# Kernel tuning notes

Measured on AMD Instinct MI355X. Metric: run time of the kernel, lower is better.

The kernel has to match this reference:

```python
import jax, jax.numpy as jnp
import numpy as np

NUM_HEADS = 12
NUM_LANDMARKS = 64


def iterative_inv(K, n_iter=6):
    # K: [B, H, L, L]; Newton-Schulz-style pseudo-inverse iteration
    I = jnp.eye(K.shape[-1], dtype=K.dtype)
    denom = jnp.max(jnp.sum(K, axis=-2), axis=-1)[..., None, None]  # [B,H,1,1]
    V = jnp.swapaxes(K, -1, -2) / denom
    for _ in range(n_iter):
        KV = K @ V
        V = 0.25 * V @ (13.0 * I - KV @ (15.0 * I - KV @ (7.0 * I - KV)))
    return V


def setup_inputs() -> dict:
    key = jax.random.key(0)
    k1, k2, k3, k4 = jax.random.split(key, 4)
    B, N, C = 8, 4096, 768
    x = jax.random.normal(k1, (B, N, C), dtype=jnp.float32)
    w_qkv = jax.random.normal(k2, (C, 3 * C), dtype=jnp.float32) * 0.02
    w_proj = jax.random.normal(k3, (C, C), dtype=jnp.float32) * 0.02
    b_proj = jax.random.normal(k4, (C,), dtype=jnp.float32) * 0.02
    return {"x": x, "w_qkv": w_qkv, "w_proj": w_proj, "b_proj": b_proj}


def reference(x, w_qkv, w_proj, b_proj):
    B, N, C = x.shape
    H, L = NUM_HEADS, NUM_LANDMARKS
    D = C // H
    scale = D ** 0.5

    qkv = (x @ w_qkv).reshape(B, N, 3, H, D)
    qkv = jnp.transpose(qkv, (2, 0, 3, 1, 4))  # [3, B, H, N, D]
    Q, K, V = qkv[0] / scale, qkv[1], qkv[2]

    segs = N // L  # r == 0 path (N divisible by L)
    K_lm = K.reshape(B, H, L, segs, D).mean(axis=-2)  # [B,H,L,D]
    Q_lm = Q.reshape(B, H, L, segs, D).mean(axis=-2)

    kernel1 = jax.nn.softmax(jnp.einsum('bhnd,bhld->bhnl', Q, K_lm), axis=-1)   # [B,H,N,L]
    kernel2 = jax.nn.softmax(jnp.einsum('bhld,bhmd->bhlm', Q_lm, K_lm), axis=-1)  # [B,H,L,L]
    kernel3 = jax.nn.softmax(jnp.einsum('bhld,bhnd->bhln', Q_lm, K), axis=-1)   # [B,H,L,N]

    SV = (kernel1 @ iterative_inv(kernel2)) @ (kernel3 @ V)  # [B,H,N,D]

    SV = jnp.transpose(SV, (0, 2, 1, 3)).reshape(B, N, C)
    out = SV @ w_proj + b_proj
    out = out + jnp.transpose(V, (0, 2, 1, 3)).reshape(B, N, C)
    return out
```

## Files before the change

kernel.cpp:

```cpp
#include <hip/hip_runtime.h>
#include <math.h>

#define BB   8
#define NN   4096
#define CC   768
#define HH   12
#define DD   64
#define LL   64
#define BH   96
#define MM_  32768
#define KQKV 768
#define NQKV 2304
#define NTILES 24

typedef short bf16x8 __attribute__((ext_vector_type(8)));
typedef float f32x4  __attribute__((ext_vector_type(4)));

union U4 { unsigned long long ll; unsigned short s[4]; };

__device__ __forceinline__ unsigned short f2bf(float f) {
  union { float f; unsigned u; } v; v.f = f;
  return (unsigned short)((v.u + 0x7FFFu + ((v.u >> 16) & 1u)) >> 16);
}
__device__ __forceinline__ float bf2f(unsigned short h) {
  union { unsigned u; float f; } v; v.u = ((unsigned)h) << 16;
  return v.f;
}
__device__ __forceinline__ f32x4 fzero4() {
  f32x4 z; z[0] = 0.f; z[1] = 0.f; z[2] = 0.f; z[3] = 0.f; return z;
}
__device__ __forceinline__ void gload_lds16(const void* g, void* l) {
  __builtin_amdgcn_global_load_lds(
      (const __attribute__((address_space(1))) void*)g,
      (__attribute__((address_space(3))) void*)l, 16, 0, 0);
}

__global__ void conv_bf16(const float* __restrict__ in, short* __restrict__ out, int n4) {
  int i = blockIdx.x * 256 + threadIdx.x;
  if (i >= n4) return;
  float4 v = ((const float4*)in)[i];
  U4 p; p.s[0] = f2bf(v.x); p.s[1] = f2bf(v.y); p.s[2] = f2bf(v.z); p.s[3] = f2bf(v.w);
  ((unsigned long long*)out)[i] = p.ll;
}

__global__ __launch_bounds__(256) void transpose_bf16(
    const float* __restrict__ in, short* __restrict__ out, int R, int C) {
  __shared__ float tile[32][33];
  int c0 = blockIdx.x * 32, r0 = blockIdx.y * 32;
  int tx = threadIdx.x & 31, ty = threadIdx.x >> 5;
  for (int i = ty; i < 32; i += 8)
    tile[i][tx] = in[(r0 + i) * C + c0 + tx];
  __syncthreads();
  for (int i = ty; i < 32; i += 8)
    out[(c0 + i) * R + r0 + tx] = (short)f2bf(tile[tx][i]);
}

template <int EPI>
__global__ __launch_bounds__(256, 3) void gemm128(
    const short* __restrict__ A, const short* __restrict__ Bw,
    short* __restrict__ o0, short* __restrict__ o1, short* __restrict__ o2,
    const float* __restrict__ bias, float* __restrict__ fout,
    short* __restrict__ Qlmb, short* __restrict__ Klmb,
    float* __restrict__ QlmF, float* __restrict__ KlmF) {
  __shared__ short L[24576];
  const int t = threadIdx.x;
  const int wave = t >> 6, lane = t & 63;
  const int wr = (wave >> 1) << 6, wc = (wave & 1) << 6;
  const int lrow = lane & 15, g = lane >> 4;

  const int q8 = gridDim.x >> 3;
  const int wg = ((int)blockIdx.x & 7) * q8 + ((int)blockIdx.x >> 3);
  const int NT = (EPI == 0) ? 18 : 6;
  const int tn = wg % NT, tm = wg / NT;
  const int m0 = tm << 7;

  const int csl = (((t & 3) ^ ((t >> 3) & 3)) << 3);
  const short* pA0 = A  + (size_t)(m0 + (t >> 2)) * KQKV + csl;
  const short* pA1 = pA0 + 64 * KQKV;
  const short* pB0 = Bw + (size_t)(tn * 128 + (t >> 2)) * KQKV + csl;
  const short* pB1 = pB0 + 64 * KQKV;
  char* dA = (char*)L + t * 16;
  char* dB = (char*)L + 8192 + t * 16;

  const int swz = ((g ^ ((lrow >> 1) & 3)) << 4);
  const int aoff = (wr + lrow) * 64 + swz;
  const int boff = 8192 + (wc + lrow) * 64 + swz;

  f32x4 acc[4][4];
#pragma unroll
  for (int i = 0; i < 4; ++i)
#pragma unroll
    for (int j = 0; j < 4; ++j) acc[i][j] = fzero4();

#pragma unroll
  for (int T = 0; T < 2; ++T) {
    gload_lds16(pA0 + T * 32, dA + T * 16384);
    gload_lds16(pA1 + T * 32, dA + T * 16384 + 4096);
    gload_lds16(pB0 + T * 32, dB + T * 16384);
    gload_lds16(pB1 + T * 32, dB + T * 16384 + 4096);
  }
  asm volatile("s_waitcnt vmcnt(4)" ::: "memory");
  __builtin_amdgcn_s_barrier();

  for (int T = 0; T < NTILES; ++T) {
    const int Ts = T + 2;
    if (Ts < NTILES) {
      const int sb = (Ts % 3) * 16384;
      gload_lds16(pA0 + Ts * 32, dA + sb);
      gload_lds16(pA1 + Ts * 32, dA + sb + 4096);
      gload_lds16(pB0 + Ts * 32, dB + sb);
      gload_lds16(pB1 + Ts * 32, dB + sb + 4096);
    }
    const char* Lb = (const char*)L + (T % 3) * 16384;
    bf16x8 a[4], b[4];
#pragma unroll
    for (int nf = 0; nf < 4; ++nf) b[nf] = *(const bf16x8*)(Lb + boff + nf * 1024);
#pragma unroll
    for (int rf = 0; rf < 4; ++rf) a[rf] = *(const bf16x8*)(Lb + aoff + rf * 1024);
#pragma unroll
    for (int rf = 0; rf < 4; ++rf)
#pragma unroll
      for (int nf = 0; nf < 4; ++nf)
        acc[rf][nf] = __builtin_amdgcn_mfma_f32_16x16x32_bf16(a[rf], b[nf], acc[rf][nf], 0, 0, 0);
    if (T < NTILES - 2)       { asm volatile("s_waitcnt vmcnt(4)" ::: "memory"); }
    else if (T == NTILES - 2) { asm volatile("s_waitcnt vmcnt(0)" ::: "memory"); }
    __builtin_amdgcn_s_barrier();
  }

  if constexpr (EPI == 0) {
    const int cg0 = tn * 128;
    const int three = cg0 / 768;
    const int ccb = cg0 % 768;
    short* dst = (three == 0) ? o0 : (three == 1) ? o1 : o2;
    const float sc = (three == 0) ? 0.125f : 1.f;
    short* LS = (short*)L;
#pragma unroll
    for (int rf = 0; rf < 4; ++rf)
#pragma unroll
      for (int nf = 0; nf < 4; ++nf)
#pragma unroll
        for (int i = 0; i < 4; ++i)
          LS[(wr + rf * 16 + g * 4 + i) * 144 + wc + nf * 16 + lrow] =
              (short)f2bf(acc[rf][nf][i] * sc);
    __syncthreads();
#pragma unroll
    for (int k = 0; k < 8; ++k) {
      int id = t + k * 256;
      int row = id >> 4, ch = id & 15;
      bf16x8 v = *(const bf16x8*)&LS[row * 144 + ch * 8];
      int c = ccb + ch * 8, h = c >> 6, d = c & 63;
      int r = m0 + row, bb = r >> 12, n = r & 4095;
      *(bf16x8*)&dst[((size_t)(bb * HH + h) * NN + n) * DD + d] = v;
    }
    if (three < 2) {
      int seg = t >> 7, col = t & 127;
      float ssum = 0.f;
#pragma unroll
      for (int j = 0; j < 64; ++j) ssum += bf2f((unsigned short)LS[(seg * 64 + j) * 144 + col]);
      ssum *= (1.f / 64.f);
      int l = ((tm & 31) << 1) + seg;
      int c = ccb + col, h = c >> 6, d = c & 63;
      int bh = (tm >> 5) * HH + h;
      int idx = bh * 4096 + l * 64 + d;
      if (three == 0) { QlmF[idx] = ssum; Qlmb[idx] = (short)f2bf(ssum); }
      else            { KlmF[idx] = ssum; Klmb[idx] = (short)f2bf(ssum); }
    }
  } else {
    float* LF = (float*)L;
#pragma unroll
    for (int pass = 0; pass < 2; ++pass) {
      if ((wave >> 1) == pass) {
#pragma unroll
        for (int rf = 0; rf < 4; ++rf)
#pragma unroll
          for (int nf = 0; nf < 4; ++nf)
#pragma unroll
            for (int i = 0; i < 4; ++i)
              LF[(rf * 16 + g * 4 + i) * 136 + wc + nf * 16 + lrow] = acc[rf][nf][i];
      }
      __syncthreads();
#pragma unroll
      for (int k = 0; k < 8; ++k) {
        int id = t + k * 256;
        int row = id >> 5, ch = id & 31;
        float4 v = *(const float4*)&LF[row * 136 + ch * 4];
        int R = m0 + pass * 64 + row;
        int c = tn * 128 + ch * 4;
        int bb = R >> 12, n = R & 4095, h = c >> 6, d = c & 63;
        float4 bi = *(const float4*)&bias[c];
        U4 r4;
        r4.ll = *(const unsigned long long*)&o2[((size_t)(bb * HH + h) * NN + n) * DD + d];
        v.x += bi.x + bf2f(r4.s[0]);
        v.y += bi.y + bf2f(r4.s[1]);
        v.z += bi.z + bf2f(r4.s[2]);
        v.w += bi.w + bf2f(r4.s[3]);
        *(float4*)&fout[(size_t)R * CC + c] = v;
      }
      __syncthreads();
    }
  }
}

__global__ __launch_bounds__(256) void e12(
    const short* __restrict__ Kb, const short* __restrict__ Vb,
    const short* __restrict__ Qlmb,
    float* __restrict__ k3VTp, float* __restrict__ s3part) {
  int bh = blockIdx.y, chunk = blockIdx.x;
  __shared__ short Qlm[64 * 72];
  __shared__ short Plds[64 * 136];
  __shared__ short Vl[128 * 68];
  int t = threadIdx.x;
  for (int r = 0; r < 2; r++) {
    int e = t + r * 256;
    *(bf16x8*)&Qlm[(e >> 3) * 72 + (e & 7) * 8] = *(const bf16x8*)&Qlmb[bh * 4096 + e * 8];
  }
  int wave = t >> 6, lane = t & 63, lrow = lane & 15, g = lane >> 4, lk = g << 3;
  f32x4 o2[4];
  float cpl[4];
#pragma unroll
  for (int lf = 0; lf < 4; lf++) { o2[lf] = fzero4(); cpl[lf] = 0.f; }
  const int dloc = wave * 16 + lrow;

  for (int s = 0; s < 4; ++s) {
    int nb = chunk * 512 + s * 128;
    __syncthreads();
#pragma unroll
    for (int r = 0; r < 4; r++) {
      int id = t + r * 256;
      int n = id >> 3, c8 = id & 7;
      unsigned long long v1 = *(const unsigned long long*)&Vb[((size_t)bh * NN + nb + n) * DD + c8 * 8];
      unsigned long long v2 = *(const unsigned long long*)&Vb[((size_t)bh * NN + nb + n) * DD + c8 * 8 + 4];
      *(unsigned long long*)&Vl[n * 68 + c8 * 8] = v1;
      *(unsigned long long*)&Vl[n * 68 + c8 * 8 + 4] = v2;
    }
    int nw = nb + wave * 32;
    bf16x8 aK[2][2];
#pragma unroll
    for (int rf = 0; rf < 2; rf++)
#pragma unroll
      for (int ks = 0; ks < 2; ks++)
        aK[rf][ks] = *(const bf16x8*)&Kb[((size_t)bh * NN + nw + rf * 16 + lrow) * DD + ks * 32 + lk];
    f32x4 acc[2][4];
#pragma unroll
    for (int rf = 0; rf < 2; rf++)
#pragma unroll
      for (int lf = 0; lf < 4; lf++) acc[rf][lf] = fzero4();
#pragma unroll
    for (int ks = 0; ks < 2; ks++) {
      bf16x8 bq[4];
#pragma unroll
      for (int lf = 0; lf < 4; lf++)
        bq[lf] = *(const bf16x8*)&Qlm[(lf * 16 + lrow) * 72 + ks * 32 + lk];
#pragma unroll
      for (int rf = 0; rf < 2; rf++)
#pragma unroll
        for (int lf = 0; lf < 4; lf++)
          acc[rf][lf] = __builtin_amdgcn_mfma_f32_16x16x32_bf16(aK[rf][ks], bq[lf], acc[rf][lf], 0, 0, 0);
    }
#pragma unroll
    for (int lf = 0; lf < 4; lf++) {
      int l = lf * 16 + lrow;
#pragma unroll
      for (int rf = 0; rf < 2; rf++) {
        U4 p;
#pragma unroll
        for (int i = 0; i < 4; i++) {
          float e = expf(acc[rf][lf][i]);
          p.s[i] = f2bf(e); cpl[lf] += e;
        }
        *(unsigned long long*)&Plds[l * 136 + wave * 32 + rf * 16 + g * 4] = p.ll;
      }
    }
    __syncthreads();
#pragma unroll
    for (int ks = 0; ks < 4; ++ks) {
      bf16x8 a;
#pragma unroll
      for (int j = 0; j < 8; ++j) a[j] = Vl[(ks * 32 + lk + j) * 68 + dloc];
#pragma unroll
      for (int lf = 0; lf < 4; lf++) {
        bf16x8 b = *(const bf16x8*)&Plds[(lf * 16 + lrow) * 136 + ks * 32 + lk];
        o2[lf] = __builtin_amdgcn_mfma_f32_16x16x32_bf16(a, b, o2[lf], 0, 0, 0);
      }
    }
  }
#pragma unroll
  for (int lf = 0; lf < 4; lf++) {
    float cp = cpl[lf];
    cp += __shfl_xor(cp, 16);
    cp += __shfl_xor(cp, 32);
    if (lane < 16)
      s3part[((bh * 8 + chunk) * 4 + wave) * LL + lf * 16 + lane] = cp;
    int l = lf * 16 + lrow;
#pragma unroll
    for (int i = 0; i < 4; i++) {
      int dd = wave * 16 + g * 4 + i;
      k3VTp[((size_t)chunk * BH + bh) * 4096 + dd * 64 + l] = o2[lf][i];
    }
  }
}

__device__ __forceinline__ void mm64(const float* X, const float* Y, int row, int c0, float o[8]) {
#pragma unroll
  for (int j = 0; j < 8; j++) o[j] = 0.f;
  for (int k = 0; k < 64; k++) {
    float x = X[row * 68 + k];
    const float4* yp = (const float4*)&Y[k * 68 + c0];
    float4 y0 = yp[0], y1 = yp[1];
    o[0] += x * y0.x; o[1] += x * y0.y; o[2] += x * y0.z; o[3] += x * y0.w;
    o[4] += x * y1.x; o[5] += x * y1.y; o[6] += x * y1.z; o[7] += x * y1.w;
  }
}

__global__ __launch_bounds__(512) void newton_inv(
    const float* __restrict__ QlmF, const float* __restrict__ KlmF,
    const float* __restrict__ k3VTp, const float* __restrict__ s3part,
    short* __restrict__ MTws) {
  __shared__ float A_[64 * 68], B_[64 * 68], C_[64 * 68], D_[64 * 68], E_[64 * 68];
  __shared__ float red[64];
  __shared__ float denom_s;
  int bh = blockIdx.x, t = threadIdx.x;
  int row = t >> 3, c0 = (t & 7) << 3;
#pragma unroll
  for (int i = 0; i < 8; i++) {
    int e = t * 8 + i;
    A_[(e >> 6) * 68 + (e & 63)] = QlmF[bh * 4096 + e];
    B_[(e >> 6) * 68 + (e & 63)] = KlmF[bh * 4096 + e];
  }
  __syncthreads();
  {
    float4 ar[16];
#pragma unroll
    for (int q = 0; q < 16; q++) ar[q] = *(const float4*)&A_[row * 68 + q * 4];
    float o[8];
#pragma unroll
    for (int mm = 0; mm < 8; mm++) {
      const float4* br = (const float4*)&B_[(c0 + mm) * 68];
      float s = 0.f;
      for (int q = 0; q < 16; q++) {
        float4 b4 = br[q];
        s += ar[q].x * b4.x + ar[q].y * b4.y + ar[q].z * b4.z + ar[q].w * b4.w;
      }
      o[mm] = s;
    }
    float mx = o[0];
#pragma unroll
    for (int mm = 1; mm < 8; mm++) mx = fmaxf(mx, o[mm]);
    mx = fmaxf(mx, __shfl_xor(mx, 1));
    mx = fmaxf(mx, __shfl_xor(mx, 2));
    mx = fmaxf(mx, __shfl_xor(mx, 4));
    float ss = 0.f;
#pragma unroll
    for (int mm = 0; mm < 8; mm++) { o[mm] = expf(o[mm] - mx); ss += o[mm]; }
    ss += __shfl_xor(ss, 1); ss += __shfl_xor(ss, 2); ss += __shfl_xor(ss, 4);
    float r = 1.f / ss;
#pragma unroll
    for (int mm = 0; mm < 8; mm++) C_[row * 68 + c0 + mm] = o[mm] * r;
  }
  __syncthreads();
  if (t < 64) {
    float s = 0.f;
    for (int l2 = 0; l2 < 64; l2++) s += C_[l2 * 68 + t];
    red[t] = s;
  }
  __syncthreads();
  if (t == 0) {
    float m = red[0];
    for (int i = 1; i < 64; i++) m = fmaxf(m, red[i]);
    denom_s = m;
  }
  __syncthreads();
  {
    float rdn = 1.f / denom_s;
#pragma unroll
    for (int i = 0; i < 8; i++) D_[row * 68 + c0 + i] = C_[(c0 + i) * 68 + row] * rdn;
  }
  __syncthreads();
  float* Vc = D_;
  float* t1 = A_;
  float* t2 = B_;
  float* t3 = E_;
  float o[8];
  for (int it = 0; it < 6; it++) {
    mm64(C_, Vc, row, c0, o);
#pragma unroll
    for (int j = 0; j < 8; j++) t1[row * 68 + c0 + j] = o[j];
    __syncthreads();
    mm64(t1, t1, row, c0, o);
#pragma unroll
    for (int j = 0; j < 8; j++) t2[row * 68 + c0 + j] = 7.f * t1[row * 68 + c0 + j] - o[j];
    __syncthreads();
    mm64(t1, t2, row, c0, o);
#pragma unroll
    for (int j = 0; j < 8; j++) t3[row * 68 + c0 + j] = 15.f * t1[row * 68 + c0 + j] - o[j];
    __syncthreads();
    mm64(Vc, t3, row, c0, o);
#pragma unroll
    for (int j = 0; j < 8; j++) t2[row * 68 + c0 + j] = 0.25f * (13.f * Vc[row * 68 + c0 + j] - o[j]);
    __syncthreads();
    float* tmp = Vc; Vc = t2; t2 = tmp;
  }
  if (t < 64) {
    float s = 0.f;
    for (int i2 = 0; i2 < 32; i2++) s += s3part[(bh * 32 + i2) * LL + t];
    red[t] = 1.f / s;
  }
  __syncthreads();
#pragma unroll
  for (int i = 0; i < 8; i++) {
    int e = t * 8 + i;
    float s = 0.f;
#pragma unroll
    for (int c = 0; c < 8; c++) s += k3VTp[((size_t)c * BH + bh) * 4096 + e];
    t1[(e >> 6) * 68 + (e & 63)] = s * red[e & 63];
  }
  __syncthreads();
  {
    float4 ar[16];
#pragma unroll
    for (int q = 0; q < 16; q++) ar[q] = *(const float4*)&t1[row * 68 + q * 4];
    for (int jj = 0; jj < 8; jj++) {
      const float4* dr = (const float4*)&Vc[(c0 + jj) * 68];
      float s = 0.f;
      for (int q = 0; q < 16; q++) {
        float4 d4 = dr[q];
        s += ar[q].x * d4.x + ar[q].y * d4.y + ar[q].z * d4.z + ar[q].w * d4.w;
      }
      MTws[bh * 4096 + row * 64 + c0 + jj] = (short)f2bf(s);
    }
  }
}

__global__ __launch_bounds__(256) void pass2(
    const short* __restrict__ Qb, const short* __restrict__ Klmb,
    const short* __restrict__ MTws, short* __restrict__ SVb) {
  int bh = blockIdx.y, n0 = blockIdx.x * 128;
  int bb = bh / HH, hh = bh % HH;
  __shared__ short Klm[64 * 72];
  __shared__ short Mt[64 * 72];
  __shared__ short Pl[128 * 72];
  int t = threadIdx.x;
  for (int r = 0; r < 2; r++) {
    int e = t + r * 256;
    *(bf16x8*)&Klm[(e >> 3) * 72 + (e & 7) * 8] = *(const bf16x8*)&Klmb[bh * 4096 + e * 8];
    *(bf16x8*)&Mt[(e >> 3) * 72 + (e & 7) * 8]  = *(const bf16x8*)&MTws[bh * 4096 + e * 8];
  }
  __syncthreads();
  int wave = t >> 6, lane = t & 63, lrow = lane & 15, lk = (lane >> 4) << 3;
  int nw = wave * 32;
  bf16x8 aQ[2][2];
#pragma unroll
  for (int rf = 0; rf < 2; rf++)
#pragma unroll
    for (int ks = 0; ks < 2; ks++)
      aQ[rf][ks] = *(const bf16x8*)&Qb[((size_t)bh * NN + n0 + nw + rf * 16 + lrow) * DD + ks * 32 + lk];
  f32x4 s[2][4];
#pragma unroll
  for (int rf = 0; rf < 2; rf++)
#pragma unroll
    for (int jf = 0; jf < 4; jf++) s[rf][jf] = fzero4();
#pragma unroll
  for (int ks = 0; ks < 2; ks++) {
    bf16x8 bk[4];
#pragma unroll
    for (int jf = 0; jf < 4; jf++)
      bk[jf] = *(const bf16x8*)&Klm[(jf * 16 + lrow) * 72 + ks * 32 + lk];
#pragma unroll
    for (int rf = 0; rf < 2; rf++)
#pragma unroll
      for (int jf = 0; jf < 4; jf++)
        s[rf][jf] = __builtin_amdgcn_mfma_f32_16x16x32_bf16(aQ[rf][ks], bk[jf], s[rf][jf], 0, 0, 0);
  }
#pragma unroll
  for (int rf = 0; rf < 2; rf++)
#pragma unroll
    for (int i = 0; i < 4; i++) {
      float v0 = s[rf][0][i], v1 = s[rf][1][i], v2 = s[rf][2][i], v3 = s[rf][3][i];
      float mx = fmaxf(fmaxf(v0, v1), fmaxf(v2, v3));
      mx = fmaxf(mx, __shfl_xor(mx, 1));
      mx = fmaxf(mx, __shfl_xor(mx, 2));
      mx = fmaxf(mx, __shfl_xor(mx, 4));
      mx = fmaxf(mx, __shfl_xor(mx, 8));
      v0 = expf(v0 - mx); v1 = expf(v1 - mx); v2 = expf(v2 - mx); v3 = expf(v3 - mx);
      float ss = v0 + v1 + v2 + v3;
      ss += __shfl_xor(ss, 1); ss += __shfl_xor(ss, 2);
      ss += __shfl_xor(ss, 4); ss += __shfl_xor(ss, 8);
      float rr = 1.f / ss;
      int n = nw + rf * 16 + ((lane >> 4) << 2) + i;
      Pl[n * 72 + 0  + lrow] = (short)f2bf(v0 * rr);
      Pl[n * 72 + 16 + lrow] = (short)f2bf(v1 * rr);
      Pl[n * 72 + 32 + lrow] = (short)f2bf(v2 * rr);
      Pl[n * 72 + 48 + lrow] = (short)f2bf(v3 * rr);
    }
  __syncthreads();
  f32x4 o[2][4];
#pragma unroll
  for (int rf = 0; rf < 2; rf++)
#pragma unroll
    for (int df = 0; df < 4; df++) o[rf][df] = fzero4();
#pragma unroll
  for (int ks = 0; ks < 2; ks++) {
    bf16x8 aP[2];
#pragma unroll
    for (int rf = 0; rf < 2; rf++)
      aP[rf] = *(const bf16x8*)&Pl[(nw + rf * 16 + lrow) * 72 + ks * 32 + lk];
    bf16x8 bm[4];
#pragma unroll
    for (int df = 0; df < 4; df++)
      bm[df] = *(const bf16x8*)&Mt[(df * 16 + lrow) * 72 + ks * 32 + lk];
#pragma unroll
    for (int rf = 0; rf < 2; rf++)
#pragma unroll
      for (int df = 0; df < 4; df++)
        o[rf][df] = __builtin_amdgcn_mfma_f32_16x16x32_bf16(aP[rf], bm[df], o[rf][df], 0, 0, 0);
  }
#pragma unroll
  for (int rf = 0; rf < 2; rf++)
#pragma unroll
    for (int df = 0; df < 4; df++)
#pragma unroll
      for (int i = 0; i < 4; i++) {
        int n = n0 + nw + rf * 16 + ((lane >> 4) << 2) + i;
        SVb[((size_t)bb * NN + n) * CC + hh * 64 + df * 16 + lrow] = (short)f2bf(o[rf][df][i]);
      }
}

extern "C" void kernel_launch(void* const* d_in, const int* in_sizes, int n_in,
                              void* d_out, int out_size, void* d_ws, size_t ws_size,
                              hipStream_t stream) {
  const float* x      = (const float*)d_in[0];
  const float* w_qkv  = (const float*)d_in[1];
  const float* w_proj = (const float*)d_in[2];
  const float* b_proj = (const float*)d_in[3];
  float* out = (float*)d_out;

  char* p = (char*)d_ws;
  auto alloc = [&](size_t bytes) -> char* {
    char* r = p; p += (bytes + 255) & ~(size_t)255; return r;
  };
  short* xb     = (short*)alloc((size_t)MM_ * KQKV * 2);
  short* wqkvT  = (short*)alloc((size_t)NQKV * KQKV * 2);
  short* wprojT = (short*)alloc((size_t)CC * CC * 2);
  short* Qb     = (short*)alloc((size_t)BH * NN * DD * 2);
  short* Kb     = (short*)alloc((size_t)BH * NN * DD * 2);
  short* Vb     = (short*)alloc((size_t)BH * NN * DD * 2);
  short* Qlmb   = (short*)alloc((size_t)BH * LL * DD * 2);
  short* Klmb   = (short*)alloc((size_t)BH * LL * DD * 2);
  float* QlmF   = (float*)alloc((size_t)BH * LL * DD * 4);
  float* KlmF   = (float*)alloc((size_t)BH * LL * DD * 4);
  float* s3part = (float*)alloc((size_t)BH * 32 * LL * 4);
  float* k3VTp  = (float*)alloc((size_t)8 * BH * DD * LL * 4);
  short* MTws   = (short*)alloc((size_t)BH * DD * LL * 2);
  short* SVb    = (short*)alloc((size_t)MM_ * CC * 2);

  conv_bf16<<<(MM_ * KQKV / 4 + 255) / 256, 256, 0, stream>>>(x, xb, MM_ * KQKV / 4);
  transpose_bf16<<<dim3(NQKV / 32, KQKV / 32), 256, 0, stream>>>(w_qkv, wqkvT, KQKV, NQKV);
  transpose_bf16<<<dim3(CC / 32, CC / 32), 256, 0, stream>>>(w_proj, wprojT, CC, CC);
  gemm128<0><<<dim3((MM_ / 128) * (NQKV / 128)), 256, 0, stream>>>(
      xb, wqkvT, Qb, Kb, Vb, nullptr, nullptr, Qlmb, Klmb, QlmF, KlmF);
  e12<<<dim3(8, BH), 256, 0, stream>>>(Kb, Vb, Qlmb, k3VTp, s3part);
  newton_inv<<<BH, 512, 0, stream>>>(QlmF, KlmF, k3VTp, s3part, MTws);
  pass2<<<dim3(NN / 128, BH), 256, 0, stream>>>(Qb, Klmb, MTws, SVb);
  gemm128<1><<<dim3((MM_ / 128) * (CC / 128)), 256, 0, stream>>>(
      SVb, wprojT, nullptr, nullptr, Vb, b_proj, out,
      nullptr, nullptr, nullptr, nullptr);
}
```

Baseline: 383.6 us.

## Merge prep kernels into one launch and remap GEMM tiles for XCD locality

Folds the bf16 conversion of x and the two weight transposes into a single prep kernel, which removes two kernel launches and their gaps. Separately, it changes the GEMM block-to-tile mapping so that each of the 8 XCD groups (blockIdx & 7) owns a contiguous band of 32 row-tiles. For the QKV GEMM the column tiles are traversed in two phases of 9, so A rows and B columns stay resident in each XCD's L2. The new mapping relies on the grid size being exactly divisible as assumed.

Measured after the change: 376.1 us. No clear change (-2.0%).

```diff
diff --git a/kernel.cpp b/kernel.cpp
--- a/kernel.cpp
+++ b/kernel.cpp
@@ -35,18 +35,29 @@
       (__attribute__((address_space(3))) void*)l, 16, 0, 0);
 }
 
-__global__ void conv_bf16(const float* __restrict__ in, short* __restrict__ out, int n4) {
-  int i = blockIdx.x * 256 + threadIdx.x;
-  if (i >= n4) return;
-  float4 v = ((const float4*)in)[i];
-  U4 p; p.s[0] = f2bf(v.x); p.s[1] = f2bf(v.y); p.s[2] = f2bf(v.z); p.s[3] = f2bf(v.w);
-  ((unsigned long long*)out)[i] = p.ll;
-}
-
-__global__ __launch_bounds__(256) void transpose_bf16(
-    const float* __restrict__ in, short* __restrict__ out, int R, int C) {
+__global__ __launch_bounds__(256) void prep(
+    const float* __restrict__ x, short* __restrict__ xb,
+    const float* __restrict__ w_qkv, short* __restrict__ wqkvT,
+    const float* __restrict__ w_proj, short* __restrict__ wprojT) {
   __shared__ float tile[32][33];
-  int c0 = blockIdx.x * 32, r0 = blockIdx.y * 32;
+  int bid = blockIdx.x;
+  if (bid < 24576) {
+    int i = bid * 256 + threadIdx.x;
+    float4 v = ((const float4*)x)[i];
+    U4 p; p.s[0] = f2bf(v.x); p.s[1] = f2bf(v.y); p.s[2] = f2bf(v.z); p.s[3] = f2bf(v.w);
+    ((unsigned long long*)xb)[i] = p.ll;
+    return;
+  }
+  const float* in; short* out; int R, C, c0, r0;
+  if (bid < 26304) {
+    int j = bid - 24576;
+    in = w_qkv; out = wqkvT; R = KQKV; C = NQKV;
+    c0 = (j % 72) * 32; r0 = (j / 72) * 32;
+  } else {
+    int j = bid - 26304;
+    in = w_proj; out = wprojT; R = CC; C = CC;
+    c0 = (j % 24) * 32; r0 = (j / 24) * 32;
+  }
   int tx = threadIdx.x & 31, ty = threadIdx.x >> 5;
   for (int i = ty; i < 32; i += 8)
     tile[i][tx] = in[(r0 + i) * C + c0 + tx];
@@ -68,10 +79,18 @@
   const int wr = (wave >> 1) << 6, wc = (wave & 1) << 6;
   const int lrow = lane & 15, g = lane >> 4;
 
-  const int q8 = gridDim.x >> 3;
-  const int wg = ((int)blockIdx.x & 7) * q8 + ((int)blockIdx.x >> 3);
-  const int NT = (EPI == 0) ? 18 : 6;
-  const int tn = wg % NT, tm = wg / NT;
+  const int x = (int)blockIdx.x & 7;
+  const int local = (int)blockIdx.x >> 3;
+  int tm, tn;
+  if constexpr (EPI == 0) {
+    const int phase = local / 288;
+    const int r = local % 288;
+    tm = x * 32 + r / 9;
+    tn = phase * 9 + r % 9;
+  } else {
+    tm = x * 32 + local / 6;
+    tn = local % 6;
+  }
   const int m0 = tm << 7;
 
   const int csl = (((t & 3) ^ ((t >> 3) & 3)) << 3);
@@ -553,9 +572,7 @@
   short* MTws   = (short*)alloc((size_t)BH * DD * LL * 2);
   short* SVb    = (short*)alloc((size_t)MM_ * CC * 2);
 
-  conv_bf16<<<(MM_ * KQKV / 4 + 255) / 256, 256, 0, stream>>>(x, xb, MM_ * KQKV / 4);
-  transpose_bf16<<<dim3(NQKV / 32, KQKV / 32), 256, 0, stream>>>(w_qkv, wqkvT, KQKV, NQKV);
-  transpose_bf16<<<dim3(CC / 32, CC / 32), 256, 0, stream>>>(w_proj, wprojT, CC, CC);
+  prep<<<26880, 256, 0, stream>>>(x, xb, w_qkv, wqkvT, w_proj, wprojT);
   gemm128<0><<<dim3((MM_ / 128) * (NQKV / 128)), 256, 0, stream>>>(
       xb, wqkvT, Qb, Kb, Vb, nullptr, nullptr, Qlmb, Klmb, QlmF, KlmF);
   e12<<<dim3(8, BH), 256, 0, stream>>>(Kb, Vb, Qlmb, k3VTp, s3part);
```
